# Optimization experiments

Measured on AMD Instinct MI355X. Metric: run time of the kernel, lower is better.

The kernel has to match this reference:

```python
import jax, jax.numpy as jnp
import numpy as np

DIM = 512
HEADS = 8
DIM_HEAD = 64
HIDDEN = HEADS * DIM_HEAD  # 512
B = 4
L = 2048
SCALE = DIM_HEAD ** -0.5


def setup_inputs() -> dict:
    key = jax.random.key(0)
    k1, k2, k3, k4 = jax.random.split(key, 4)
    x = jax.random.normal(k1, (B, DIM, L), dtype=jnp.float32)
    # Conv1d with kernel_size=1 == pointwise matmul over channels; store as [out, in]
    w_qkv = jax.random.normal(k2, (HIDDEN * 3, DIM), dtype=jnp.float32) * (DIM ** -0.5)
    w_out = jax.random.normal(k3, (DIM, HIDDEN), dtype=jnp.float32) * (HIDDEN ** -0.5)
    b_out = jax.random.normal(k4, (DIM,), dtype=jnp.float32) * 0.01
    return {"x": x, "w_qkv": w_qkv, "w_out": w_out, "b_out": b_out}


def reference(x, w_qkv, w_out, b_out):
    # x: [B, dim, L]
    qkv = jnp.einsum('oi,bil->bol', w_qkv, x)           # [B, 3*hidden, L]
    q, k, v = jnp.split(qkv, 3, axis=1)                  # each [B, hidden, L]

    def to_heads(t):
        # 'b (h c) l -> b h l c'
        return t.reshape(t.shape[0], HEADS, DIM_HEAD, t.shape[-1]).transpose(0, 1, 3, 2)

    q = to_heads(q) * SCALE                              # [B, H, L, c]
    k = to_heads(k)
    v = to_heads(v)

    attn = jax.nn.softmax(jnp.einsum('bhqc,bhkc->bhqk', q, k), axis=-1)  # [B,H,L,L]
    o = jnp.einsum('bhqk,bhkc->bhqc', attn, v)           # [B, H, L, c]
    o = o.transpose(0, 1, 3, 2).reshape(o.shape[0], HIDDEN, o.shape[2] if False else L)
    # 'b h c l -> b (h c) l' done via transpose+reshape above
    out = jnp.einsum('oi,bil->bol', w_out, o) + b_out[None, :, None]
    return out
```

## Files before the change

kernel.cpp:

```cpp
#include <hip/hip_runtime.h>

typedef unsigned short u16;
typedef __bf16 bf16x8 __attribute__((ext_vector_type(8)));
typedef float f32x4 __attribute__((ext_vector_type(4)));

#define B_ 4
#define L_ 2048
#define LOG2E 1.44269504088896340736f
#define HSTRIDE ((size_t)L_ * 64)

__device__ __forceinline__ u16 f2bf(float f) {
    unsigned u = __float_as_uint(f);
    u += 0x7fff + ((u >> 16) & 1);
    return (u16)(u >> 16);
}

__device__ __forceinline__ f32x4 mfma16(bf16x8 a, bf16x8 b, f32x4 c) {
    return __builtin_amdgcn_mfma_f32_16x16x32_bf16(a, b, c, 0, 0, 0);
}

__device__ __forceinline__ void async16(const u16* g, u16* l) {
    __builtin_amdgcn_global_load_lds(
        (const __attribute__((address_space(1))) u16*)g,
        (__attribute__((address_space(3))) u16*)l, 16, 0, 0);
}

__global__ __launch_bounds__(256) void convert_f32_bf16(const float* __restrict__ in,
                                                        u16* __restrict__ out, int n) {
    int i = (blockIdx.x * 256 + threadIdx.x) * 4;
    if (i < n) {
        float4 f = *(const float4*)(in + i);
        ushort4 r;
        r.x = f2bf(f.x); r.y = f2bf(f.y); r.z = f2bf(f.z); r.w = f2bf(f.w);
        *(ushort4*)(out + i) = r;
    }
}

__global__ __launch_bounds__(256) void transpose_x(const float* __restrict__ x,
                                                   u16* __restrict__ xbt) {
    __shared__ u16 T[64][66];
    int b  = blockIdx.z;
    int i0 = blockIdx.y * 64;
    int l0 = blockIdx.x * 64;
    int t  = threadIdx.x;
    int c  = t & 63, r4 = t >> 6;
    const float* xb = x + ((size_t)b * 512 + i0) * 2048 + l0;
#pragma unroll
    for (int r = r4; r < 64; r += 4) T[r][c] = f2bf(xb[(size_t)r * 2048 + c]);
    __syncthreads();
    u16* ob = xbt + ((size_t)b * 2048 + l0) * 512 + i0;
#pragma unroll
    for (int r = r4; r < 64; r += 4) ob[(size_t)r * 512 + c] = T[c][r];
}

__global__ __launch_bounds__(256, 2) void qkv_gemm(const u16* __restrict__ xbt,
                                                   const u16* __restrict__ wq,
                                                   u16* __restrict__ qkv) {
    __shared__ u16 smem[16896];
    u16* As = smem;
    u16* Bs = smem + 8192;
    int b  = blockIdx.z;
    int m0 = blockIdx.x * 128;
    int n0 = blockIdx.y * 128;
    int tid = threadIdx.x;
    int lane = tid & 63, wid = tid >> 6;
    int quad = lane >> 4, n15 = lane & 15;
    const u16* Abase = xbt + ((size_t)b * L_ + m0) * 512;
    const u16* Bbase = wq + (size_t)n0 * 512;
    int mw = (wid & 1) * 64, nw = (wid >> 1) * 64;
    f32x4 acc[4][4] = {};
    for (int k0 = 0; k0 < 512; k0 += 64) {
        __syncthreads();
#pragma unroll
        for (int c = 0; c < 4; ++c) {
            int off = wid * 2048 + c * 512 + lane * 8;
            int row = off >> 6, col = off & 63;
            async16(Abase + (size_t)row * 512 + k0 + col, As + wid * 2048 + c * 512);
            async16(Bbase + (size_t)row * 512 + k0 + col, Bs + wid * 2048 + c * 512);
        }
        __syncthreads();
#pragma unroll
        for (int ks = 0; ks < 2; ++ks) {
            bf16x8 af[4], bfr[4];
#pragma unroll
            for (int i = 0; i < 4; ++i)
                af[i] = *(const bf16x8*)&As[(mw + i * 16 + n15) * 64 + ks * 32 + quad * 8];
#pragma unroll
            for (int j = 0; j < 4; ++j)
                bfr[j] = *(const bf16x8*)&Bs[(nw + j * 16 + n15) * 64 + ks * 32 + quad * 8];
#pragma unroll
            for (int i = 0; i < 4; ++i)
#pragma unroll
                for (int j = 0; j < 4; ++j)
                    acc[i][j] = mfma16(af[i], bfr[j], acc[i][j]);
        }
    }
    if (n0 < 1024) {
#pragma unroll
        for (int i = 0; i < 4; ++i) {
#pragma unroll
            for (int j = 0; j < 4; ++j) {
                int o = n0 + nw + j * 16 + n15;
                int t = o >> 9, h = (o >> 6) & 7, cc = o & 63;
                float sc = (t == 0) ? (0.125f * LOG2E) : 1.0f;
                u16* dst = qkv + (((size_t)b * 3 + t) * 8 + h) * HSTRIDE + cc;
#pragma unroll
                for (int r = 0; r < 4; ++r) {
                    int l = m0 + mw + i * 16 + quad * 4 + r;
                    dst[(size_t)l * 64] = f2bf(acc[i][j][r] * sc);
                }
            }
        }
    } else {
        __syncthreads();
        u16* T = smem;
#pragma unroll
        for (int i = 0; i < 4; ++i)
#pragma unroll
            for (int j = 0; j < 4; ++j)
#pragma unroll
                for (int r = 0; r < 4; ++r)
                    T[(nw + j * 16 + n15) * 132 + (mw + i * 16 + quad * 4 + r)] =
                        f2bf(acc[i][j][r]);
        __syncthreads();
        int h0 = (n0 - 1024) >> 6;
        u16* Vt = qkv + ((size_t)b * 3 + 2) * 8 * HSTRIDE;
#pragma unroll
        for (int c8 = 0; c8 < 8; ++c8) {
            int off = c8 * 2048 + tid * 8;
            int cfull = off >> 7, l = off & 127;
            int h = h0 + (cfull >> 6), cc = cfull & 63;
            ushort4 lo = *(const ushort4*)&T[cfull * 132 + l];
            ushort4 hi = *(const ushort4*)&T[cfull * 132 + l + 4];
            ushort4* dst = (ushort4*)(Vt + (size_t)h * HSTRIDE + (size_t)cc * L_ + m0 + l);
            dst[0] = lo; dst[1] = hi;
        }
    }
}

__global__ __launch_bounds__(256, 2) void attn_kernel(const u16* __restrict__ qkv,
                                                      u16* __restrict__ o2) {
    __shared__ u16 Ks[128 * 64];
    __shared__ u16 Vs[64 * 128];
    __shared__ u16 Ps[128 * 140];
    int bh = blockIdx.y;
    int b = bh >> 3, h = bh & 7;
    int q0 = blockIdx.x * 128;
    int tid = threadIdx.x, lane = tid & 63, wid = tid >> 6;
    int quad = lane >> 4, n15 = lane & 15;
    const u16* Qp = qkv + (((size_t)b * 3 + 0) * 8 + h) * HSTRIDE;
    const u16* Kp = qkv + (((size_t)b * 3 + 1) * 8 + h) * HSTRIDE;
    const u16* Vt = qkv + (((size_t)b * 3 + 2) * 8 + h) * HSTRIDE;
    int mw = wid * 32;
    u16* Pw = Ps + mw * 140;

    bf16x8 aq[2][2];
#pragma unroll
    for (int mf = 0; mf < 2; ++mf)
#pragma unroll
        for (int ks = 0; ks < 2; ++ks)
            aq[mf][ks] = *(const bf16x8*)
                &Qp[(size_t)(q0 + mw + mf * 16 + n15) * 64 + ks * 32 + quad * 8];

    f32x4 oacc[2][4] = {};
    float lsum[2][4] = {};

    int kr = lane >> 3, kc = lane & 7;
    int vr = lane >> 4, vc = lane & 15;

    for (int kt = 0; kt < 16; ++kt) {
        int kl0 = kt * 128;
        __syncthreads();
#pragma unroll
        for (int c = 0; c < 4; ++c) {
            int ko = wid * 4 + c;
            int row = ko * 8 + kr;
            async16(Kp + (size_t)(kl0 + row) * 64 + ((kc ^ (row & 7)) * 8),
                    Ks + ko * 512 + lane * 8);
            int vo = wid * 4 + c;
            int crow = vo * 4 + vr;
            async16(Vt + (size_t)crow * L_ + kl0 + ((vc ^ (crow & 15)) * 8),
                    Vs + vo * 512 + lane * 8);
        }
        __syncthreads();

        f32x4 sacc[2][8] = {};
#pragma unroll
        for (int nf = 0; nf < 8; ++nf) {
#pragma unroll
            for (int ks = 0; ks < 2; ++ks) {
                int row = nf * 16 + n15;
                int ch = (ks * 4 + quad) ^ (row & 7);
                bf16x8 bk = *(const bf16x8*)&Ks[row * 64 + ch * 8];
                sacc[0][nf] = mfma16(aq[0][ks], bk, sacc[0][nf]);
                sacc[1][nf] = mfma16(aq[1][ks], bk, sacc[1][nf]);
            }
        }
#pragma unroll
        for (int mf = 0; mf < 2; ++mf)
#pragma unroll
            for (int nf = 0; nf < 8; ++nf)
#pragma unroll
                for (int r = 0; r < 4; ++r) {
                    float p = __builtin_amdgcn_exp2f(sacc[mf][nf][r]);
                    lsum[mf][r] += p;
                    Pw[(mf * 16 + quad * 4 + r) * 140 + nf * 16 + n15] = f2bf(p);
                }
#pragma unroll
        for (int ks2 = 0; ks2 < 4; ++ks2) {
            bf16x8 pa0 = *(const bf16x8*)&Pw[n15 * 140 + ks2 * 32 + quad * 8];
            bf16x8 pa1 = *(const bf16x8*)&Pw[(16 + n15) * 140 + ks2 * 32 + quad * 8];
#pragma unroll
            for (int nf2 = 0; nf2 < 4; ++nf2) {
                int crow = nf2 * 16 + n15;
                int ch = (ks2 * 4 + quad) ^ (crow & 15);
                bf16x8 vb = *(const bf16x8*)&Vs[crow * 128 + ch * 8];
                oacc[0][nf2] = mfma16(pa0, vb, oacc[0][nf2]);
                oacc[1][nf2] = mfma16(pa1, vb, oacc[1][nf2]);
            }
        }
    }
#pragma unroll
    for (int mf = 0; mf < 2; ++mf)
#pragma unroll
        for (int r = 0; r < 4; ++r) {
            float s = lsum[mf][r];
            s += __shfl_xor(s, 1, 64);
            s += __shfl_xor(s, 2, 64);
            s += __shfl_xor(s, 4, 64);
            s += __shfl_xor(s, 8, 64);
            float inv = 1.0f / s;
            int l = q0 + mw + mf * 16 + quad * 4 + r;
#pragma unroll
            for (int nf2 = 0; nf2 < 4; ++nf2) {
                int cc = nf2 * 16 + n15;
                o2[((size_t)b * L_ + l) * 512 + h * 64 + cc] = f2bf(oacc[mf][nf2][r] * inv);
            }
        }
}

__global__ __launch_bounds__(256, 2) void out_gemm(const u16* __restrict__ wo,
                                                   const u16* __restrict__ o2,
                                                   const float* __restrict__ bout,
                                                   float* __restrict__ out) {
    __shared__ u16 As[8192], Bs[8192];
    int b  = blockIdx.z;
    int m0 = blockIdx.y * 128;
    int n0 = blockIdx.x * 128;
    int tid = threadIdx.x, lane = tid & 63, wid = tid >> 6;
    int quad = lane >> 4, n15 = lane & 15;
    const u16* Abase = wo + (size_t)m0 * 512;
    const u16* Bbase = o2 + ((size_t)b * L_ + n0) * 512;
    int mw = (wid & 1) * 64, nw = (wid >> 1) * 64;
    f32x4 acc[4][4] = {};
    for (int k0 = 0; k0 < 512; k0 += 64) {
        __syncthreads();
#pragma unroll
        for (int c = 0; c < 4; ++c) {
            int off = wid * 2048 + c * 512 + lane * 8;
            int row = off >> 6, col = off & 63;
            async16(Abase + (size_t)row * 512 + k0 + col, As + wid * 2048 + c * 512);
            async16(Bbase + (size_t)row * 512 + k0 + col, Bs + wid * 2048 + c * 512);
        }
        __syncthreads();
#pragma unroll
        for (int ks = 0; ks < 2; ++ks) {
            bf16x8 af[4], bfr[4];
#pragma unroll
            for (int i = 0; i < 4; ++i)
                af[i] = *(const bf16x8*)&As[(mw + i * 16 + n15) * 64 + ks * 32 + quad * 8];
#pragma unroll
            for (int j = 0; j < 4; ++j)
                bfr[j] = *(const bf16x8*)&Bs[(nw + j * 16 + n15) * 64 + ks * 32 + quad * 8];
#pragma unroll
            for (int i = 0; i < 4; ++i)
#pragma unroll
                for (int j = 0; j < 4; ++j)
                    acc[i][j] = mfma16(af[i], bfr[j], acc[i][j]);
        }
    }
#pragma unroll
    for (int i = 0; i < 4; ++i) {
#pragma unroll
        for (int r = 0; r < 4; ++r) {
            int o_ = m0 + mw + i * 16 + quad * 4 + r;
            float bias = bout[o_];
            float* dst = out + ((size_t)b * 512 + o_) * L_ + n0;
#pragma unroll
            for (int j = 0; j < 4; ++j) dst[nw + j * 16 + n15] = acc[i][j][r] + bias;
        }
    }
}

#define OFF_XBT  ((size_t)0)
#define OFF_WQKV (OFF_XBT + (size_t)B_ * L_ * 512)
#define OFF_WOUT (OFF_WQKV + (size_t)1536 * 512)
#define OFF_QKV  (OFF_WOUT + (size_t)512 * 512)
#define OFF_O2   (OFF_QKV + (size_t)3 * B_ * 8 * L_ * 64)

extern "C" void kernel_launch(void* const* d_in, const int* in_sizes, int n_in,
                              void* d_out, int out_size, void* d_ws, size_t ws_size,
                              hipStream_t stream) {
    (void)in_sizes; (void)n_in; (void)out_size; (void)ws_size;
    const float* x    = (const float*)d_in[0];
    const float* wqkv = (const float*)d_in[1];
    const float* wout = (const float*)d_in[2];
    const float* bout = (const float*)d_in[3];
    float* out = (float*)d_out;
    u16* ws = (u16*)d_ws;
    u16* xbt   = ws + OFF_XBT;
    u16* wqkvb = ws + OFF_WQKV;
    u16* woutb = ws + OFF_WOUT;
    u16* qkv   = ws + OFF_QKV;
    u16* o2    = ws + OFF_O2;

    convert_f32_bf16<<<768, 256, 0, stream>>>(wqkv, wqkvb, 1536 * 512);
    convert_f32_bf16<<<256, 256, 0, stream>>>(wout, woutb, 512 * 512);
    transpose_x<<<dim3(32, 8, 4), 256, 0, stream>>>(x, xbt);
    qkv_gemm<<<dim3(16, 12, 4), 256, 0, stream>>>(xbt, wqkvb, qkv);
    attn_kernel<<<dim3(16, 32), 256, 0, stream>>>(qkv, o2);
    out_gemm<<<dim3(16, 4, 4), 256, 0, stream>>>(woutb, o2, bout, out);
}
```

Measured before the change: 191.3 us.

## Store K in MFMA fragment layout and compute transposed scores from global

The QKV GEMM epilogue now writes K pre-swizzled into the per-lane MFMA operand layout, so the attention kernel loads K fragments directly from global memory with coalesced 16-byte loads instead of staging K through LDS. Scores are computed transposed (K as the A operand), which lets each lane pack four consecutive probabilities into one ushort4 LDS store and keep a single running sum per fragment, reduced with cross-quad shuffles at the end. This removes the K LDS buffer, its async copies and the per-element P stores, at the cost of K global-load latency sitting on the critical path inside the inner loop, with no LDS reuse across waves.

```diff
diff --git a/kernel.cpp b/kernel.cpp
--- a/kernel.cpp
+++ b/kernel.cpp
@@ -95,19 +95,36 @@
                     acc[i][j] = mfma16(af[i], bfr[j], acc[i][j]);
         }
     }
-    if (n0 < 1024) {
+    if (n0 < 512) {
 #pragma unroll
         for (int i = 0; i < 4; ++i) {
 #pragma unroll
             for (int j = 0; j < 4; ++j) {
                 int o = n0 + nw + j * 16 + n15;
-                int t = o >> 9, h = (o >> 6) & 7, cc = o & 63;
-                float sc = (t == 0) ? (0.125f * LOG2E) : 1.0f;
-                u16* dst = qkv + (((size_t)b * 3 + t) * 8 + h) * HSTRIDE + cc;
+                int h = (o >> 6) & 7, cc = o & 63;
+                u16* dst = qkv + ((size_t)b * 3 * 8 + h) * HSTRIDE + cc;
 #pragma unroll
                 for (int r = 0; r < 4; ++r) {
                     int l = m0 + mw + i * 16 + quad * 4 + r;
-                    dst[(size_t)l * 64] = f2bf(acc[i][j][r] * sc);
+                    dst[(size_t)l * 64] = f2bf(acc[i][j][r] * (0.125f * LOG2E));
+                }
+            }
+        }
+    } else if (n0 < 1024) {
+#pragma unroll
+        for (int i = 0; i < 4; ++i) {
+            int tile = (m0 + mw + i * 16) >> 4;
+#pragma unroll
+            for (int j = 0; j < 4; ++j) {
+                int o = n0 + nw + j * 16 + n15;
+                int h = (o >> 6) & 7, c = o & 63;
+                int ks_k = c >> 5, qk = (c >> 3) & 3, jj = c & 7;
+                u16* dst = qkv + (((size_t)b * 3 + 1) * 8 + h) * HSTRIDE
+                         + ((size_t)tile * 2 + ks_k) * 512 + qk * 128 + jj;
+#pragma unroll
+                for (int r = 0; r < 4; ++r) {
+                    int n15k = quad * 4 + r;
+                    dst[n15k * 8] = f2bf(acc[i][j][r]);
                 }
             }
         }
@@ -140,7 +157,6 @@
 
 __global__ __launch_bounds__(256, 2) void attn_kernel(const u16* __restrict__ qkv,
                                                       u16* __restrict__ o2) {
-    __shared__ u16 Ks[128 * 64];
     __shared__ u16 Vs[64 * 128];
     __shared__ u16 Ps[128 * 140];
     int bh = blockIdx.y;
@@ -149,7 +165,7 @@
     int tid = threadIdx.x, lane = tid & 63, wid = tid >> 6;
     int quad = lane >> 4, n15 = lane & 15;
     const u16* Qp = qkv + (((size_t)b * 3 + 0) * 8 + h) * HSTRIDE;
-    const u16* Kp = qkv + (((size_t)b * 3 + 1) * 8 + h) * HSTRIDE;
+    const u16* Kf = qkv + (((size_t)b * 3 + 1) * 8 + h) * HSTRIDE;
     const u16* Vt = qkv + (((size_t)b * 3 + 2) * 8 + h) * HSTRIDE;
     int mw = wid * 32;
     u16* Pw = Ps + mw * 140;
@@ -163,9 +179,8 @@
                 &Qp[(size_t)(q0 + mw + mf * 16 + n15) * 64 + ks * 32 + quad * 8];
 
     f32x4 oacc[2][4] = {};
-    float lsum[2][4] = {};
-
-    int kr = lane >> 3, kc = lane & 7;
+    float lsumT[2] = {0.f, 0.f};
+
     int vr = lane >> 4, vc = lane & 15;
 
     for (int kt = 0; kt < 16; ++kt) {
@@ -173,10 +188,6 @@
         __syncthreads();
 #pragma unroll
         for (int c = 0; c < 4; ++c) {
-            int ko = wid * 4 + c;
-            int row = ko * 8 + kr;
-            async16(Kp + (size_t)(kl0 + row) * 64 + ((kc ^ (row & 7)) * 8),
-                    Ks + ko * 512 + lane * 8);
             int vo = wid * 4 + c;
             int crow = vo * 4 + vr;
             async16(Vt + (size_t)crow * L_ + kl0 + ((vc ^ (crow & 15)) * 8),
@@ -184,28 +195,28 @@
         }
         __syncthreads();
 
-        f32x4 sacc[2][8] = {};
 #pragma unroll
         for (int nf = 0; nf < 8; ++nf) {
+            f32x4 sT[2] = {};
 #pragma unroll
             for (int ks = 0; ks < 2; ++ks) {
-                int row = nf * 16 + n15;
-                int ch = (ks * 4 + quad) ^ (row & 7);
-                bf16x8 bk = *(const bf16x8*)&Ks[row * 64 + ch * 8];
-                sacc[0][nf] = mfma16(aq[0][ks], bk, sacc[0][nf]);
-                sacc[1][nf] = mfma16(aq[1][ks], bk, sacc[1][nf]);
-            }
-        }
-#pragma unroll
-        for (int mf = 0; mf < 2; ++mf)
-#pragma unroll
-            for (int nf = 0; nf < 8; ++nf)
-#pragma unroll
-                for (int r = 0; r < 4; ++r) {
-                    float p = __builtin_amdgcn_exp2f(sacc[mf][nf][r]);
-                    lsum[mf][r] += p;
-                    Pw[(mf * 16 + quad * 4 + r) * 140 + nf * 16 + n15] = f2bf(p);
-                }
+                bf16x8 ak = *(const bf16x8*)
+                    &Kf[(size_t)((kt * 8 + nf) * 2 + ks) * 512 + lane * 8];
+                sT[0] = mfma16(ak, aq[0][ks], sT[0]);
+                sT[1] = mfma16(ak, aq[1][ks], sT[1]);
+            }
+#pragma unroll
+            for (int mf = 0; mf < 2; ++mf) {
+                float p0 = __builtin_amdgcn_exp2f(sT[mf][0]);
+                float p1 = __builtin_amdgcn_exp2f(sT[mf][1]);
+                float p2 = __builtin_amdgcn_exp2f(sT[mf][2]);
+                float p3 = __builtin_amdgcn_exp2f(sT[mf][3]);
+                lsumT[mf] += (p0 + p1) + (p2 + p3);
+                ushort4 pk;
+                pk.x = f2bf(p0); pk.y = f2bf(p1); pk.z = f2bf(p2); pk.w = f2bf(p3);
+                *(ushort4*)&Pw[(mf * 16 + n15) * 140 + nf * 16 + quad * 4] = pk;
+            }
+        }
 #pragma unroll
         for (int ks2 = 0; ks2 < 4; ++ks2) {
             bf16x8 pa0 = *(const bf16x8*)&Pw[n15 * 140 + ks2 * 32 + quad * 8];
@@ -220,16 +231,21 @@
             }
         }
     }
+    float inv_[2][4];
+#pragma unroll
+    for (int mf = 0; mf < 2; ++mf) {
+        float s = lsumT[mf];
+        s += __shfl_xor(s, 16, 64);
+        s += __shfl_xor(s, 32, 64);
+#pragma unroll
+        for (int r = 0; r < 4; ++r)
+            inv_[mf][r] = 1.0f / __shfl(s, (lane & 48) | (quad * 4 + r), 64);
+    }
 #pragma unroll
     for (int mf = 0; mf < 2; ++mf)
 #pragma unroll
         for (int r = 0; r < 4; ++r) {
-            float s = lsum[mf][r];
-            s += __shfl_xor(s, 1, 64);
-            s += __shfl_xor(s, 2, 64);
-            s += __shfl_xor(s, 4, 64);
-            s += __shfl_xor(s, 8, 64);
-            float inv = 1.0f / s;
+            float inv = inv_[mf][r];
             int l = q0 + mw + mf * 16 + quad * 4 + r;
 #pragma unroll
             for (int nf2 = 0; nf2 < 4; ++nf2) {
```

New measurement: 208.8 us. 1.09x slower.
